# Kernel tuning notes

Hardware: AMD Instinct MI355X
Metric: run time of the kernel (lower is better)

Reference implementation:

```python
import jax, jax.numpy as jnp
import numpy as np

B, S, E, H = 2, 2048, 768, 8
D = E // H  # 96
SCALING = D ** (-0.5)


def setup_inputs() -> dict:
    key = jax.random.key(0)
    ks = jax.random.split(key, 7)
    sd = E ** -0.5
    return {
        "x": jax.random.normal(ks[0], (B, S, E), jnp.float32),
        "Wq": jax.random.normal(ks[1], (E, E), jnp.float32) * sd,
        "bq": jax.random.normal(ks[2], (E,), jnp.float32) * 0.02,
        "Wk": jax.random.normal(ks[3], (E, E), jnp.float32) * sd,
        "bk": jax.random.normal(ks[4], (E,), jnp.float32) * 0.02,
        "Wo": jax.random.normal(ks[5], (E, E), jnp.float32) * sd,
        "bo": jax.random.normal(ks[6], (E,), jnp.float32) * 0.02,
    }


def _split_heads(t):
    # [B, S, E] -> [B, H, S, D]
    return t.reshape(B, S, H, D).transpose(0, 2, 1, 3)


def reference(x, Wq, bq, Wk, bk, Wo, bo):
    q = _split_heads(x @ Wq + bq)
    k = _split_heads(x @ Wk + bk)
    # NOTE: faithful to source bug — values use the KEY projection
    v = _split_heads(x @ Wk + bk)
    energies = jnp.einsum("bhqd,bhkd->bhqk", q, k)  # [B,H,S,S]
    # NOTE: faithful to source — scaling applied AFTER softmax
    attn = jax.nn.softmax(energies, axis=-1) * SCALING
    out = jnp.einsum("bhqk,bhkd->bhqd", attn, v)
    out = out.transpose(0, 2, 1, 3).reshape(B, S, E)
    return out @ Wo + bo
```

## Files before the change

### kernel.cpp

```cpp
#include <hip/hip_runtime.h>
#include <hip/hip_bf16.h>
#include <math.h>
#include <stdint.h>

#define B_DIM 2
#define S_DIM 2048
#define E_DIM 768
#define H_DIM 8
#define D_DIM 96
#define M_DIM (B_DIM*S_DIM)
#define SCALE_F 0.10206207261596575f

typedef _Float16 f16x8 __attribute__((ext_vector_type(8)));
typedef float    f32x4  __attribute__((ext_vector_type(4)));
typedef float    f32x16 __attribute__((ext_vector_type(16)));

#define MFMA16H(a,b,c) __builtin_amdgcn_mfma_f32_16x16x32_f16(a,b,c,0,0,0)
#define MFMA32H(a,b,c) __builtin_amdgcn_mfma_f32_32x32x16_f16(a,b,c,0,0,0)

__device__ inline unsigned short f2h(float f) {
    return __builtin_bit_cast(unsigned short, (_Float16)f);
}

__device__ inline void gload16(const void* g, void* l) {
    auto gp = reinterpret_cast<const __attribute__((address_space(1))) uint32_t*>(
        reinterpret_cast<uintptr_t>(g));
    auto lp = reinterpret_cast<__attribute__((address_space(3))) uint32_t*>(
        reinterpret_cast<uintptr_t>(l));
    __builtin_amdgcn_global_load_lds(gp, lp, 16, 0, 0);
}

__global__ __launch_bounds__(256) void convert_x_kernel(
    const float* __restrict__ X, unsigned short* __restrict__ Xf)
{
    int i = (blockIdx.x * 256 + threadIdx.x) * 4;
    float4 v = *(const float4*)(X + i);
    ushort4 h;
    h.x = f2h(v.x); h.y = f2h(v.y); h.z = f2h(v.z); h.w = f2h(v.w);
    *(ushort4*)(Xf + i) = h;
}

__global__ __launch_bounds__(256) void convert_wT3_kernel(
    const float* __restrict__ W0, const float* __restrict__ W1,
    const float* __restrict__ W2,
    unsigned short* __restrict__ T0, unsigned short* __restrict__ T1,
    unsigned short* __restrict__ T2)
{
    const float* W; unsigned short* T;
    if (blockIdx.z == 0)      { W = W0; T = T0; }
    else if (blockIdx.z == 1) { W = W1; T = T1; }
    else                      { W = W2; T = T2; }

    __shared__ float tile[64][65];
    const int tid = threadIdx.x;
    const int k0 = blockIdx.y << 6, n0 = blockIdx.x << 6;
    const int r = tid >> 4, c4 = (tid & 15) << 2;
    #pragma unroll
    for (int i = 0; i < 4; ++i) {
        float4 v = *(const float4*)(W + (size_t)(k0 + r + i*16)*E_DIM + n0 + c4);
        tile[r + i*16][c4+0] = v.x; tile[r + i*16][c4+1] = v.y;
        tile[r + i*16][c4+2] = v.z; tile[r + i*16][c4+3] = v.w;
    }
    __syncthreads();
    #pragma unroll
    for (int i = 0; i < 4; ++i) {
        int n = r + i*16;
        ushort4 h;
        h.x = f2h(tile[c4+0][n]); h.y = f2h(tile[c4+1][n]);
        h.z = f2h(tile[c4+2][n]); h.w = f2h(tile[c4+3][n]);
        *(ushort4*)(T + (size_t)(n0 + n)*E_DIM + k0 + c4) = h;
    }
}

__global__ __launch_bounds__(256) void gemm_qk_kernel(
    const unsigned short* __restrict__ A, const unsigned short* __restrict__ Bt,
    const float* __restrict__ bq, const float* __restrict__ bk,
    unsigned short* __restrict__ Qf, unsigned short* __restrict__ Kf)
{
    __shared__ unsigned short sA[128*32];
    __shared__ unsigned short sB[128*32];

    const int tid  = threadIdx.x;
    const int lane = tid & 63;
    const int w    = tid >> 6;
    const int qn   = lane & 15, quad = lane >> 4;
    const int wm   = w & 1, wn = w >> 1;
    const int row0 = blockIdx.y << 7;
    const int col0 = blockIdx.x << 7;

    const int sr = tid >> 2;
    const int sk = (tid & 3) << 3;

    const unsigned short* gA = A  + (size_t)(row0 + sr)*E_DIM + sk;
    const unsigned short* gB = Bt + (size_t)(col0 + sr)*E_DIM + sk;

    f32x4 acc[4][4];
    #pragma unroll
    for (int mt = 0; mt < 4; ++mt)
        #pragma unroll
        for (int nt = 0; nt < 4; ++nt)
            { acc[mt][nt][0]=0.f; acc[mt][nt][1]=0.f; acc[mt][nt][2]=0.f; acc[mt][nt][3]=0.f; }

    for (int k0 = 0; k0 < E_DIM; k0 += 32) {
        __syncthreads();
        gload16(gA + k0,            sA + tid*8);
        gload16(gA + 64*E_DIM + k0, sA + 2048 + tid*8);
        gload16(gB + k0,            sB + tid*8);
        gload16(gB + 64*E_DIM + k0, sB + 2048 + tid*8);
        __syncthreads();

        f16x8 af[4], bf[4];
        #pragma unroll
        for (int mt = 0; mt < 4; ++mt)
            af[mt] = *(const f16x8*)&sA[(wm*64 + mt*16 + qn)*32 + quad*8];
        #pragma unroll
        for (int nt = 0; nt < 4; ++nt)
            bf[nt] = *(const f16x8*)&sB[(wn*64 + nt*16 + qn)*32 + quad*8];
        #pragma unroll
        for (int mt = 0; mt < 4; ++mt)
            #pragma unroll
            for (int nt = 0; nt < 4; ++nt)
                acc[mt][nt] = MFMA16H(af[mt], bf[nt], acc[mt][nt]);
    }

    #pragma unroll
    for (int nt = 0; nt < 4; ++nt) {
        int n = col0 + wn*64 + nt*16 + qn;
        bool isQ = n < E_DIM;
        float bias = isQ ? bq[n] : bk[n - E_DIM];
        unsigned short* op = isQ ? Qf : Kf;
        int nc = isQ ? n : n - E_DIM;
        #pragma unroll
        for (int mt = 0; mt < 4; ++mt)
            #pragma unroll
            for (int r = 0; r < 4; ++r) {
                int m = row0 + wm*64 + mt*16 + quad*4 + r;
                op[(size_t)m*E_DIM + nc] = f2h(acc[mt][nt][r] + bias);
            }
    }
}

__global__ __launch_bounds__(256) void gemm_out_kernel(
    const unsigned short* __restrict__ A, const unsigned short* __restrict__ Bt,
    const float* __restrict__ bo, float* __restrict__ out)
{
    __shared__ unsigned short sA[128*32];
    __shared__ unsigned short sB[64*32];

    const int tid  = threadIdx.x;
    const int lane = tid & 63;
    const int w    = tid >> 6;
    const int qn   = lane & 15, quad = lane >> 4;
    const int wm   = w & 1, wn = w >> 1;
    const int row0 = blockIdx.y << 7;
    const int col0 = blockIdx.x << 6;

    const int sr = tid >> 2;
    const int sk = (tid & 3) << 3;

    const unsigned short* gA = A  + (size_t)(row0 + sr)*E_DIM + sk;
    const unsigned short* gB = Bt + (size_t)(col0 + sr)*E_DIM + sk;

    f32x4 acc[4][2];
    #pragma unroll
    for (int mt = 0; mt < 4; ++mt)
        #pragma unroll
        for (int nt = 0; nt < 2; ++nt)
            { acc[mt][nt][0]=0.f; acc[mt][nt][1]=0.f; acc[mt][nt][2]=0.f; acc[mt][nt][3]=0.f; }

    for (int k0 = 0; k0 < E_DIM; k0 += 32) {
        __syncthreads();
        gload16(gA + k0,            sA + tid*8);
        gload16(gA + 64*E_DIM + k0, sA + 2048 + tid*8);
        gload16(gB + k0,            sB + tid*8);
        __syncthreads();

        f16x8 af[4], bf[2];
        #pragma unroll
        for (int mt = 0; mt < 4; ++mt)
            af[mt] = *(const f16x8*)&sA[(wm*64 + mt*16 + qn)*32 + quad*8];
        #pragma unroll
        for (int nt = 0; nt < 2; ++nt)
            bf[nt] = *(const f16x8*)&sB[(wn*32 + nt*16 + qn)*32 + quad*8];
        #pragma unroll
        for (int mt = 0; mt < 4; ++mt)
            #pragma unroll
            for (int nt = 0; nt < 2; ++nt)
                acc[mt][nt] = MFMA16H(af[mt], bf[nt], acc[mt][nt]);
    }

    #pragma unroll
    for (int nt = 0; nt < 2; ++nt) {
        int n = col0 + wn*32 + nt*16 + qn;
        float bias = bo[n];
        #pragma unroll
        for (int mt = 0; mt < 4; ++mt)
            #pragma unroll
            for (int r = 0; r < 4; ++r) {
                int m = row0 + wm*64 + mt*16 + quad*4 + r;
                out[(size_t)m*E_DIM + n] = acc[mt][nt][r] + bias;
            }
    }
}

__global__ __launch_bounds__(256) void attn_mfma_kernel(
    const unsigned short* __restrict__ Qf, const unsigned short* __restrict__ Kf,
    unsigned short* __restrict__ O0, unsigned short* __restrict__ O1,
    float2* __restrict__ ml)
{
    __shared__ unsigned short sKh[64][104];
    __shared__ unsigned short sKt[96][72];
    __shared__ unsigned short sPs[128][72];

    const int tid  = threadIdx.x;
    const int w    = tid >> 6;
    const int lane = tid & 63;
    const int col  = lane & 31;
    const int half = lane >> 5;
    const int b    = blockIdx.z >> 1;
    const int kh   = blockIdx.z & 1;
    const int h    = blockIdx.y;
    const int q0   = blockIdx.x << 7;
    const int key0 = kh << 10;

    f16x8 qf[6];
    {
        const size_t ro = ((size_t)(b*S_DIM + q0 + w*32 + col))*E_DIM
                          + h*D_DIM + half*8;
        #pragma unroll
        for (int kc = 0; kc < 6; ++kc)
            qf[kc] = *(const f16x8*)(Qf + ro + kc*16);
    }

    f32x16 o[3];
    #pragma unroll
    for (int nt = 0; nt < 3; ++nt)
        #pragma unroll
        for (int r = 0; r < 16; ++r) o[nt][r] = 0.f;
    float m_i = -INFINITY, l_i = 0.f;

    const bool stager = tid < 128;
    const int st = tid & 127;
    const int sp = st >> 2;
    const int dq = st & 3;

    uint4 r0[3], r1[3];
    if (stager) {
        const size_t g0 = ((size_t)(b*S_DIM + key0 + 2*sp))*E_DIM + h*D_DIM + dq*24;
        #pragma unroll
        for (int i = 0; i < 3; ++i) {
            r0[i] = *(const uint4*)(Kf + g0 + 8*i);
            r1[i] = *(const uint4*)(Kf + g0 + E_DIM + 8*i);
        }
    }

    for (int kt = 0; kt < 16; ++kt) {
        __syncthreads();
        if (stager) {
            #pragma unroll
            for (int i = 0; i < 3; ++i) {
                *(uint4*)&sKh[2*sp  ][dq*24 + 8*i] = r0[i];
                *(uint4*)&sKh[2*sp+1][dq*24 + 8*i] = r1[i];
            }
            const unsigned short* p0 = (const unsigned short*)r0;
            const unsigned short* p1 = (const unsigned short*)r1;
            #pragma unroll
            for (int c = 0; c < 24; ++c) {
                unsigned int pk = (unsigned int)p0[c] | ((unsigned int)p1[c] << 16);
                *(unsigned int*)&sKt[dq*24 + c][2*sp] = pk;
            }
        }
        __syncthreads();

        if (stager && kt + 1 < 16) {
            const size_t g0 = ((size_t)(b*S_DIM + key0 + (kt+1)*64 + 2*sp))*E_DIM
                              + h*D_DIM + dq*24;
            #pragma unroll
            for (int i = 0; i < 3; ++i) {
                r0[i] = *(const uint4*)(Kf + g0 + 8*i);
                r1[i] = *(const uint4*)(Kf + g0 + E_DIM + 8*i);
            }
        }

        f32x16 s[2];
        #pragma unroll
        for (int mt = 0; mt < 2; ++mt) {
            f32x16 acc;
            #pragma unroll
            for (int r = 0; r < 16; ++r) acc[r] = 0.f;
            #pragma unroll
            for (int kc = 0; kc < 6; ++kc) {
                f16x8 ah = *(const f16x8*)&sKh[mt*32 + col][kc*16 + half*8];
                acc = MFMA32H(ah, qf[kc], acc);
            }
            s[mt] = acc;
        }

        float mx = s[0][0];
        #pragma unroll
        for (int mt = 0; mt < 2; ++mt)
            #pragma unroll
            for (int r = 0; r < 16; ++r) mx = fmaxf(mx, s[mt][r]);
        mx = fmaxf(mx, __shfl_xor(mx, 32));

        float m_new = fmaxf(m_i, mx);
        float alpha = __expf(m_i - m_new);
        m_i = m_new;

        float psum = 0.f;
        #pragma unroll
        for (int mt = 0; mt < 2; ++mt)
            #pragma unroll
            for (int g = 0; g < 4; ++g) {
                float e0 = __expf(s[mt][4*g+0] - m_new);
                float e1 = __expf(s[mt][4*g+1] - m_new);
                float e2 = __expf(s[mt][4*g+2] - m_new);
                float e3 = __expf(s[mt][4*g+3] - m_new);
                psum += e0 + e1 + e2 + e3;
                ushort4 pk;
                pk.x = f2h(e0); pk.y = f2h(e1); pk.z = f2h(e2); pk.w = f2h(e3);
                *(ushort4*)&sPs[w*32 + col][mt*32 + 8*g + 4*half] = pk;
            }
        psum += __shfl_xor(psum, 32);
        l_i = l_i * alpha + psum;

        #pragma unroll
        for (int g = 0; g < 4; ++g)
            #pragma unroll
            for (int r = 0; r < 4; ++r) {
                float ar = __shfl(alpha, 8*g + r + 4*half);
                #pragma unroll
                for (int nt = 0; nt < 3; ++nt) o[nt][4*g + r] *= ar;
            }

        #pragma unroll
        for (int kc = 0; kc < 4; ++kc) {
            f16x8 pa = *(const f16x8*)&sPs[w*32 + col][kc*16 + half*8];
            #pragma unroll
            for (int nt = 0; nt < 3; ++nt) {
                f16x8 vb = *(const f16x8*)&sKt[nt*32 + col][kc*16 + half*8];
                o[nt] = MFMA32H(pa, vb, o[nt]);
            }
        }
    }

    unsigned short* Ob = (kh ? O1 : O0)
        + ((size_t)(b*S_DIM + q0 + w*32))*E_DIM + h*D_DIM;
    #pragma unroll
    for (int g = 0; g < 4; ++g)
        #pragma unroll
        for (int r = 0; r < 4; ++r) {
            int qr = 8*g + r + 4*half;
            #pragma unroll
            for (int nt = 0; nt < 3; ++nt)
                Ob[(size_t)qr*E_DIM + nt*32 + col] = f2h(o[nt][4*g + r]);
        }
    if (lane < 32) {
        int q = q0 + w*32 + lane;
        ml[((size_t)(kh*B_DIM + b)*H_DIM + h)*S_DIM + q] = make_float2(m_i, l_i);
    }
}

__global__ __launch_bounds__(256) void combine_kernel(
    const unsigned short* __restrict__ O0, const unsigned short* __restrict__ O1,
    const float2* __restrict__ ml, unsigned short* __restrict__ ctx)
{
    size_t idx = ((size_t)blockIdx.x * 256 + threadIdx.x) * 4;
    int row = (int)(idx / E_DIM);
    int ce  = (int)(idx % E_DIM);
    int h   = ce / D_DIM;
    int b   = row >> 11;
    int q   = row & (S_DIM - 1);

    float2 m0 = ml[((size_t)(0*B_DIM + b)*H_DIM + h)*S_DIM + q];
    float2 m1 = ml[((size_t)(1*B_DIM + b)*H_DIM + h)*S_DIM + q];
    float m  = fmaxf(m0.x, m1.x);
    float w0 = __expf(m0.x - m), w1 = __expf(m1.x - m);
    float l  = m0.y * w0 + m1.y * w1;
    float s0 = w0 * SCALE_F / l, s1 = w1 * SCALE_F / l;

    ushort4 a = *(const ushort4*)(O0 + idx);
    ushort4 c = *(const ushort4*)(O1 + idx);
    ushort4 o;
    o.x = f2h((float)__builtin_bit_cast(_Float16, a.x)*s0 + (float)__builtin_bit_cast(_Float16, c.x)*s1);
    o.y = f2h((float)__builtin_bit_cast(_Float16, a.y)*s0 + (float)__builtin_bit_cast(_Float16, c.y)*s1);
    o.z = f2h((float)__builtin_bit_cast(_Float16, a.z)*s0 + (float)__builtin_bit_cast(_Float16, c.z)*s1);
    o.w = f2h((float)__builtin_bit_cast(_Float16, a.w)*s0 + (float)__builtin_bit_cast(_Float16, c.w)*s1);
    *(ushort4*)(ctx + idx) = o;
}

extern "C" void kernel_launch(void* const* d_in, const int* in_sizes, int n_in,
                              void* d_out, int out_size, void* d_ws, size_t ws_size,
                              hipStream_t stream)
{
    const float* x  = (const float*)d_in[0];
    const float* Wq = (const float*)d_in[1];
    const float* bq = (const float*)d_in[2];
    const float* Wk = (const float*)d_in[3];
    const float* bk = (const float*)d_in[4];
    const float* Wo = (const float*)d_in[5];
    const float* bo = (const float*)d_in[6];
    float* out = (float*)d_out;

    const size_t NE = (size_t)M_DIM * E_DIM;
    const size_t WE = (size_t)E_DIM * E_DIM;
    unsigned short* xf   = (unsigned short*)d_ws;
    unsigned short* WqkT = xf + NE;
    unsigned short* WoT  = WqkT + 2*WE;
    unsigned short* Qf   = WoT + WE;
    unsigned short* Kf   = Qf + NE;
    unsigned short* ctx  = Kf + NE;
    float2*         mlbuf = (float2*)(ctx + NE);
    unsigned short* Oh0  = xf;
    unsigned short* Oh1  = (unsigned short*)d_out;

    dim3 blk(256);
    hipLaunchKernelGGL(convert_x_kernel, dim3(NE/1024), blk, 0, stream, x, xf);
    hipLaunchKernelGGL(convert_wT3_kernel, dim3(12,12,3), blk, 0, stream,
                       Wq, Wk, Wo, WqkT, WqkT + WE, WoT);

    hipLaunchKernelGGL(gemm_qk_kernel, dim3(12,32), blk, 0, stream,
                       xf, WqkT, bq, bk, Qf, Kf);

    hipLaunchKernelGGL(attn_mfma_kernel, dim3(S_DIM/128, H_DIM, B_DIM*2), blk, 0,
                       stream, Qf, Kf, Oh0, Oh1, mlbuf);

    hipLaunchKernelGGL(combine_kernel, dim3(NE/1024), blk, 0, stream,
                       Oh0, Oh1, mlbuf, ctx);

    hipLaunchKernelGGL(gemm_out_kernel, dim3(12,32), blk, 0, stream,
                       ctx, WoT, bo, out);
}
```

Baseline: 168.3 us.

## Fuse split-KV combine into output GEMM and use exp2 softmax

The standalone combine pass over both partial attention outputs is removed. A small kernel now computes per-row, per-head merge weights, and the output GEMM applies them while staging its A tile into LDS, with the next tile's loads issued early in registers. The output GEMM tile grows to 128x128 (6x32 blocks), Q is prescaled by log2e so softmax can use exp2, and the attention kernel swaps MFMA operand order so each lane owns a query row. That removes the alpha shuffles and lets the output store use vectorized ushort4 writes. In exchange the A-tile path loses the async global-to-LDS load, and the grid for the output GEMM has fewer blocks.

```diff
diff --git a/kernel.cpp b/kernel.cpp
--- a/kernel.cpp
+++ b/kernel.cpp
@@ -10,6 +10,7 @@
 #define D_DIM 96
 #define M_DIM (B_DIM*S_DIM)
 #define SCALE_F 0.10206207261596575f
+#define LOG2E_F 1.4426950408889634f
 
 typedef _Float16 f16x8 __attribute__((ext_vector_type(8)));
 typedef float    f32x4  __attribute__((ext_vector_type(4)));
@@ -20,6 +21,9 @@
 
 __device__ inline unsigned short f2h(float f) {
     return __builtin_bit_cast(unsigned short, (_Float16)f);
+}
+__device__ inline float h2f(unsigned short u) {
+    return (float)__builtin_bit_cast(_Float16, u);
 }
 
 __device__ inline void gload16(const void* g, void* l) {
@@ -128,6 +132,7 @@
         int n = col0 + wn*64 + nt*16 + qn;
         bool isQ = n < E_DIM;
         float bias = isQ ? bq[n] : bk[n - E_DIM];
+        float post = isQ ? LOG2E_F : 1.0f;
         unsigned short* op = isQ ? Qf : Kf;
         int nc = isQ ? n : n - E_DIM;
         #pragma unroll
@@ -135,70 +140,7 @@
             #pragma unroll
             for (int r = 0; r < 4; ++r) {
                 int m = row0 + wm*64 + mt*16 + quad*4 + r;
-                op[(size_t)m*E_DIM + nc] = f2h(acc[mt][nt][r] + bias);
-            }
-    }
-}
-
-__global__ __launch_bounds__(256) void gemm_out_kernel(
-    const unsigned short* __restrict__ A, const unsigned short* __restrict__ Bt,
-    const float* __restrict__ bo, float* __restrict__ out)
-{
-    __shared__ unsigned short sA[128*32];
-    __shared__ unsigned short sB[64*32];
-
-    const int tid  = threadIdx.x;
-    const int lane = tid & 63;
-    const int w    = tid >> 6;
-    const int qn   = lane & 15, quad = lane >> 4;
-    const int wm   = w & 1, wn = w >> 1;
-    const int row0 = blockIdx.y << 7;
-    const int col0 = blockIdx.x << 6;
-
-    const int sr = tid >> 2;
-    const int sk = (tid & 3) << 3;
-
-    const unsigned short* gA = A  + (size_t)(row0 + sr)*E_DIM + sk;
-    const unsigned short* gB = Bt + (size_t)(col0 + sr)*E_DIM + sk;
-
-    f32x4 acc[4][2];
-    #pragma unroll
-    for (int mt = 0; mt < 4; ++mt)
-        #pragma unroll
-        for (int nt = 0; nt < 2; ++nt)
-            { acc[mt][nt][0]=0.f; acc[mt][nt][1]=0.f; acc[mt][nt][2]=0.f; acc[mt][nt][3]=0.f; }
-
-    for (int k0 = 0; k0 < E_DIM; k0 += 32) {
-        __syncthreads();
-        gload16(gA + k0,            sA + tid*8);
-        gload16(gA + 64*E_DIM + k0, sA + 2048 + tid*8);
-        gload16(gB + k0,            sB + tid*8);
-        __syncthreads();
-
-        f16x8 af[4], bf[2];
-        #pragma unroll
-        for (int mt = 0; mt < 4; ++mt)
-            af[mt] = *(const f16x8*)&sA[(wm*64 + mt*16 + qn)*32 + quad*8];
-        #pragma unroll
-        for (int nt = 0; nt < 2; ++nt)
-            bf[nt] = *(const f16x8*)&sB[(wn*32 + nt*16 + qn)*32 + quad*8];
-        #pragma unroll
-        for (int mt = 0; mt < 4; ++mt)
-            #pragma unroll
-            for (int nt = 0; nt < 2; ++nt)
-                acc[mt][nt] = MFMA16H(af[mt], bf[nt], acc[mt][nt]);
-    }
-
-    #pragma unroll
-    for (int nt = 0; nt < 2; ++nt) {
-        int n = col0 + wn*32 + nt*16 + qn;
-        float bias = bo[n];
-        #pragma unroll
-        for (int mt = 0; mt < 4; ++mt)
-            #pragma unroll
-            for (int r = 0; r < 4; ++r) {
-                int m = row0 + wm*64 + mt*16 + quad*4 + r;
-                out[(size_t)m*E_DIM + n] = acc[mt][nt][r] + bias;
+                op[(size_t)m*E_DIM + nc] = f2h((acc[mt][nt][r] + bias) * post);
             }
     }
 }
@@ -304,7 +246,7 @@
         mx = fmaxf(mx, __shfl_xor(mx, 32));
 
         float m_new = fmaxf(m_i, mx);
-        float alpha = __expf(m_i - m_new);
+        float alpha = exp2f(m_i - m_new);
         m_i = m_new;
 
         float psum = 0.f;
@@ -312,10 +254,10 @@
         for (int mt = 0; mt < 2; ++mt)
             #pragma unroll
             for (int g = 0; g < 4; ++g) {
-                float e0 = __expf(s[mt][4*g+0] - m_new);
-                float e1 = __expf(s[mt][4*g+1] - m_new);
-                float e2 = __expf(s[mt][4*g+2] - m_new);
-                float e3 = __expf(s[mt][4*g+3] - m_new);
+                float e0 = exp2f(s[mt][4*g+0] - m_new);
+                float e1 = exp2f(s[mt][4*g+1] - m_new);
+                float e2 = exp2f(s[mt][4*g+2] - m_new);
+                float e3 = exp2f(s[mt][4*g+3] - m_new);
                 psum += e0 + e1 + e2 + e3;
                 ushort4 pk;
                 pk.x = f2h(e0); pk.y = f2h(e1); pk.z = f2h(e2); pk.w = f2h(e3);
@@ -325,35 +267,31 @@
         l_i = l_i * alpha + psum;
 
         #pragma unroll
-        for (int g = 0; g < 4; ++g)
-            #pragma unroll
-            for (int r = 0; r < 4; ++r) {
-                float ar = __shfl(alpha, 8*g + r + 4*half);
-                #pragma unroll
-                for (int nt = 0; nt < 3; ++nt) o[nt][4*g + r] *= ar;
-            }
+        for (int nt = 0; nt < 3; ++nt)
+            #pragma unroll
+            for (int r = 0; r < 16; ++r) o[nt][r] *= alpha;
 
         #pragma unroll
         for (int kc = 0; kc < 4; ++kc) {
-            f16x8 pa = *(const f16x8*)&sPs[w*32 + col][kc*16 + half*8];
+            f16x8 pb = *(const f16x8*)&sPs[w*32 + col][kc*16 + half*8];
             #pragma unroll
             for (int nt = 0; nt < 3; ++nt) {
-                f16x8 vb = *(const f16x8*)&sKt[nt*32 + col][kc*16 + half*8];
-                o[nt] = MFMA32H(pa, vb, o[nt]);
+                f16x8 va = *(const f16x8*)&sKt[nt*32 + col][kc*16 + half*8];
+                o[nt] = MFMA32H(va, pb, o[nt]);
             }
         }
     }
 
     unsigned short* Ob = (kh ? O1 : O0)
-        + ((size_t)(b*S_DIM + q0 + w*32))*E_DIM + h*D_DIM;
-    #pragma unroll
-    for (int g = 0; g < 4; ++g)
-        #pragma unroll
-        for (int r = 0; r < 4; ++r) {
-            int qr = 8*g + r + 4*half;
-            #pragma unroll
-            for (int nt = 0; nt < 3; ++nt)
-                Ob[(size_t)qr*E_DIM + nt*32 + col] = f2h(o[nt][4*g + r]);
+        + ((size_t)(b*S_DIM + q0 + w*32 + col))*E_DIM + h*D_DIM;
+    #pragma unroll
+    for (int nt = 0; nt < 3; ++nt)
+        #pragma unroll
+        for (int rg = 0; rg < 4; ++rg) {
+            ushort4 pk;
+            pk.x = f2h(o[nt][4*rg+0]); pk.y = f2h(o[nt][4*rg+1]);
+            pk.z = f2h(o[nt][4*rg+2]); pk.w = f2h(o[nt][4*rg+3]);
+            *(ushort4*)(Ob + nt*32 + 8*rg + 4*half) = pk;
         }
     if (lane < 32) {
         int q = q0 + w*32 + lane;
@@ -361,32 +299,127 @@
     }
 }
 
-__global__ __launch_bounds__(256) void combine_kernel(
+__global__ __launch_bounds__(256) void scale_kernel(
+    const float2* __restrict__ ml, float2* __restrict__ sc)
+{
+    int idx = blockIdx.x * 256 + threadIdx.x;
+    int m = idx >> 3, h = idx & 7;
+    int b = m >> 11, q = m & (S_DIM - 1);
+    float2 e0 = ml[((size_t)(0*B_DIM + b)*H_DIM + h)*S_DIM + q];
+    float2 e1 = ml[((size_t)(1*B_DIM + b)*H_DIM + h)*S_DIM + q];
+    float mm = fmaxf(e0.x, e1.x);
+    float w0 = exp2f(e0.x - mm), w1 = exp2f(e1.x - mm);
+    float l = e0.y*w0 + e1.y*w1;
+    float inv = SCALE_F / l;
+    sc[idx] = make_float2(w0*inv, w1*inv);
+}
+
+__global__ __launch_bounds__(256) void gemm_out_kernel(
     const unsigned short* __restrict__ O0, const unsigned short* __restrict__ O1,
-    const float2* __restrict__ ml, unsigned short* __restrict__ ctx)
-{
-    size_t idx = ((size_t)blockIdx.x * 256 + threadIdx.x) * 4;
-    int row = (int)(idx / E_DIM);
-    int ce  = (int)(idx % E_DIM);
-    int h   = ce / D_DIM;
-    int b   = row >> 11;
-    int q   = row & (S_DIM - 1);
-
-    float2 m0 = ml[((size_t)(0*B_DIM + b)*H_DIM + h)*S_DIM + q];
-    float2 m1 = ml[((size_t)(1*B_DIM + b)*H_DIM + h)*S_DIM + q];
-    float m  = fmaxf(m0.x, m1.x);
-    float w0 = __expf(m0.x - m), w1 = __expf(m1.x - m);
-    float l  = m0.y * w0 + m1.y * w1;
-    float s0 = w0 * SCALE_F / l, s1 = w1 * SCALE_F / l;
-
-    ushort4 a = *(const ushort4*)(O0 + idx);
-    ushort4 c = *(const ushort4*)(O1 + idx);
-    ushort4 o;
-    o.x = f2h((float)__builtin_bit_cast(_Float16, a.x)*s0 + (float)__builtin_bit_cast(_Float16, c.x)*s1);
-    o.y = f2h((float)__builtin_bit_cast(_Float16, a.y)*s0 + (float)__builtin_bit_cast(_Float16, c.y)*s1);
-    o.z = f2h((float)__builtin_bit_cast(_Float16, a.z)*s0 + (float)__builtin_bit_cast(_Float16, c.z)*s1);
-    o.w = f2h((float)__builtin_bit_cast(_Float16, a.w)*s0 + (float)__builtin_bit_cast(_Float16, c.w)*s1);
-    *(ushort4*)(ctx + idx) = o;
+    const float2* __restrict__ sc, const unsigned short* __restrict__ Bt,
+    const float* __restrict__ bo, float* __restrict__ out)
+{
+    __shared__ unsigned short sA[128*32];
+    __shared__ unsigned short sB[128*32];
+
+    const int tid  = threadIdx.x;
+    const int lane = tid & 63;
+    const int w    = tid >> 6;
+    const int qn   = lane & 15, quad = lane >> 4;
+    const int wm   = w & 1, wn = w >> 1;
+    const int row0 = blockIdx.y << 7;
+    const int col0 = blockIdx.x << 7;
+
+    const int sr = tid >> 2;
+    const int sk = (tid & 3) << 3;
+
+    const size_t r0o = (size_t)(row0 + sr)*E_DIM;
+    const size_t r1o = (size_t)(row0 + sr + 64)*E_DIM;
+    const unsigned short* gB = Bt + (size_t)(col0 + sr)*E_DIM + sk;
+
+    f32x4 acc[4][4];
+    #pragma unroll
+    for (int mt = 0; mt < 4; ++mt)
+        #pragma unroll
+        for (int nt = 0; nt < 4; ++nt)
+            { acc[mt][nt][0]=0.f; acc[mt][nt][1]=0.f; acc[mt][nt][2]=0.f; acc[mt][nt][3]=0.f; }
+
+    ushort4 u0a, u0b, u1a, u1b, v0a, v0b, v1a, v1b;
+    float2 s0, s1;
+    {
+        u0a = *(const ushort4*)(O0 + r0o + sk);     u0b = *(const ushort4*)(O0 + r0o + sk + 4);
+        u1a = *(const ushort4*)(O0 + r1o + sk);     u1b = *(const ushort4*)(O0 + r1o + sk + 4);
+        v0a = *(const ushort4*)(O1 + r0o + sk);     v0b = *(const ushort4*)(O1 + r0o + sk + 4);
+        v1a = *(const ushort4*)(O1 + r1o + sk);     v1b = *(const ushort4*)(O1 + r1o + sk + 4);
+        s0  = sc[(size_t)(row0 + sr)*H_DIM];
+        s1  = sc[(size_t)(row0 + sr + 64)*H_DIM];
+    }
+
+    for (int k0 = 0; k0 < E_DIM; k0 += 32) {
+        __syncthreads();
+        {
+            ushort4 h0a, h0b, h1a, h1b;
+            h0a.x = f2h(fmaf(h2f(v0a.x), s0.y, h2f(u0a.x)*s0.x));
+            h0a.y = f2h(fmaf(h2f(v0a.y), s0.y, h2f(u0a.y)*s0.x));
+            h0a.z = f2h(fmaf(h2f(v0a.z), s0.y, h2f(u0a.z)*s0.x));
+            h0a.w = f2h(fmaf(h2f(v0a.w), s0.y, h2f(u0a.w)*s0.x));
+            h0b.x = f2h(fmaf(h2f(v0b.x), s0.y, h2f(u0b.x)*s0.x));
+            h0b.y = f2h(fmaf(h2f(v0b.y), s0.y, h2f(u0b.y)*s0.x));
+            h0b.z = f2h(fmaf(h2f(v0b.z), s0.y, h2f(u0b.z)*s0.x));
+            h0b.w = f2h(fmaf(h2f(v0b.w), s0.y, h2f(u0b.w)*s0.x));
+            h1a.x = f2h(fmaf(h2f(v1a.x), s1.y, h2f(u1a.x)*s1.x));
+            h1a.y = f2h(fmaf(h2f(v1a.y), s1.y, h2f(u1a.y)*s1.x));
+            h1a.z = f2h(fmaf(h2f(v1a.z), s1.y, h2f(u1a.z)*s1.x));
+            h1a.w = f2h(fmaf(h2f(v1a.w), s1.y, h2f(u1a.w)*s1.x));
+            h1b.x = f2h(fmaf(h2f(v1b.x), s1.y, h2f(u1b.x)*s1.x));
+            h1b.y = f2h(fmaf(h2f(v1b.y), s1.y, h2f(u1b.y)*s1.x));
+            h1b.z = f2h(fmaf(h2f(v1b.z), s1.y, h2f(u1b.z)*s1.x));
+            h1b.w = f2h(fmaf(h2f(v1b.w), s1.y, h2f(u1b.w)*s1.x));
+            *(ushort4*)&sA[sr*32 + sk]            = h0a;
+            *(ushort4*)&sA[sr*32 + sk + 4]        = h0b;
+            *(ushort4*)&sA[(sr + 64)*32 + sk]     = h1a;
+            *(ushort4*)&sA[(sr + 64)*32 + sk + 4] = h1b;
+        }
+        gload16(gB + k0,            sB + tid*8);
+        gload16(gB + 64*E_DIM + k0, sB + 2048 + tid*8);
+        __syncthreads();
+
+        if (k0 + 32 < E_DIM) {
+            int kn = k0 + 32;
+            u0a = *(const ushort4*)(O0 + r0o + kn + sk); u0b = *(const ushort4*)(O0 + r0o + kn + sk + 4);
+            u1a = *(const ushort4*)(O0 + r1o + kn + sk); u1b = *(const ushort4*)(O0 + r1o + kn + sk + 4);
+            v0a = *(const ushort4*)(O1 + r0o + kn + sk); v0b = *(const ushort4*)(O1 + r0o + kn + sk + 4);
+            v1a = *(const ushort4*)(O1 + r1o + kn + sk); v1b = *(const ushort4*)(O1 + r1o + kn + sk + 4);
+            s0  = sc[(size_t)(row0 + sr)*H_DIM + kn/D_DIM];
+            s1  = sc[(size_t)(row0 + sr + 64)*H_DIM + kn/D_DIM];
+        }
+
+        f16x8 af[4], bf[4];
+        #pragma unroll
+        for (int mt = 0; mt < 4; ++mt)
+            af[mt] = *(const f16x8*)&sA[(wm*64 + mt*16 + qn)*32 + quad*8];
+        #pragma unroll
+        for (int nt = 0; nt < 4; ++nt)
+            bf[nt] = *(const f16x8*)&sB[(wn*64 + nt*16 + qn)*32 + quad*8];
+        #pragma unroll
+        for (int mt = 0; mt < 4; ++mt)
+            #pragma unroll
+            for (int nt = 0; nt < 4; ++nt)
+                acc[mt][nt] = MFMA16H(af[mt], bf[nt], acc[mt][nt]);
+    }
+
+    #pragma unroll
+    for (int nt = 0; nt < 4; ++nt) {
+        int n = col0 + wn*64 + nt*16 + qn;
+        float bias = bo[n];
+        #pragma unroll
+        for (int mt = 0; mt < 4; ++mt)
+            #pragma unroll
+            for (int r = 0; r < 4; ++r) {
+                int m = row0 + wm*64 + mt*16 + quad*4 + r;
+                out[(size_t)m*E_DIM + n] = acc[mt][nt][r] + bias;
+            }
+    }
 }
 
 extern "C" void kernel_launch(void* const* d_in, const int* in_sizes, int n_in,
@@ -404,15 +437,15 @@
 
     const size_t NE = (size_t)M_DIM * E_DIM;
     const size_t WE = (size_t)E_DIM * E_DIM;
-    unsigned short* xf   = (unsigned short*)d_ws;
-    unsigned short* WqkT = xf + NE;
-    unsigned short* WoT  = WqkT + 2*WE;
-    unsigned short* Qf   = WoT + WE;
-    unsigned short* Kf   = Qf + NE;
-    unsigned short* ctx  = Kf + NE;
-    float2*         mlbuf = (float2*)(ctx + NE);
-    unsigned short* Oh0  = xf;
-    unsigned short* Oh1  = (unsigned short*)d_out;
+    unsigned short* xf    = (unsigned short*)d_ws;
+    unsigned short* WqkT  = xf + NE;
+    unsigned short* WoT   = WqkT + 2*WE;
+    unsigned short* Qf    = WoT + WE;
+    unsigned short* Kf    = Qf + NE;
+    unsigned short* Oh1   = Kf + NE;
+    float2*         mlbuf = (float2*)(Oh1 + NE);
+    float2*         scbuf = mlbuf + 2*(size_t)B_DIM*H_DIM*S_DIM;
+    unsigned short* Oh0   = xf;
 
     dim3 blk(256);
     hipLaunchKernelGGL(convert_x_kernel, dim3(NE/1024), blk, 0, stream, x, xf);
@@ -425,9 +458,9 @@
     hipLaunchKernelGGL(attn_mfma_kernel, dim3(S_DIM/128, H_DIM, B_DIM*2), blk, 0,
                        stream, Qf, Kf, Oh0, Oh1, mlbuf);
 
-    hipLaunchKernelGGL(combine_kernel, dim3(NE/1024), blk, 0, stream,
-                       Oh0, Oh1, mlbuf, ctx);
-
-    hipLaunchKernelGGL(gemm_out_kernel, dim3(12,32), blk, 0, stream,
-                       ctx, WoT, bo, out);
-}
+    hipLaunchKernelGGL(scale_kernel, dim3(M_DIM*H_DIM/256), blk, 0, stream,
+                       mlbuf, scbuf);
+
+    hipLaunchKernelGGL(gemm_out_kernel, dim3(6,32), blk, 0, stream,
+                       Oh0, Oh1, scbuf, WoT, bo, out);
+}
```

Result: slower. 179.4 us (+6.6%).
